# Kernel tuning notes

Hardware: AMD Instinct MI355X
Metric: run time of the kernel (lower is better)

The kernel has to match this reference:

```python
import jax, jax.numpy as jnp
import numpy as np

B, S, DIM = 2, 4096, 768
G = DIM // 3          # gate_dim = 256
H, DK = 4, G // 4     # heads=4, d_k=64
SCALE = 1.0 / np.sqrt(DK)


def setup_inputs() -> dict:
    key = jax.random.key(0)
    ks = jax.random.split(key, 9)
    r = lambda k, shp, s: (jax.random.normal(k, shp, dtype=jnp.float32) * s)
    w_s = 1.0 / np.sqrt(G)
    return {
        "x": r(ks[0], (B, S, DIM), 1.0),
        "wq": r(ks[1], (G, G), w_s), "bq": r(ks[2], (G,), 0.01),
        "wk": r(ks[3], (G, G), w_s), "bk": r(ks[4], (G,), 0.01),
        "wv": r(ks[5], (G, G), w_s), "bv": r(ks[6], (G,), 0.01),
        "wo": r(ks[7], (G, G), w_s), "bo": r(ks[8], (G,), 0.01),
    }


def reference(x, wq, bq, wk, bk, wv, bv, wo, bo):
    # chunk(3, dim=-1): q/k/v slices of width G
    xq, xk, xv = x[..., :G], x[..., G:2 * G], x[..., 2 * G:3 * G]
    # linear projections then split into heads: [b, s, h, d]
    q = (xq @ wq.T + bq).reshape(B, S, H, DK)
    k = (xk @ wk.T + bk).reshape(B, S, H, DK)
    v = (xv @ wv.T + bv).reshape(B, S, H, DK)
    scores = jnp.einsum('bihd,bjhd->bijh', q, k) * SCALE  # [b, i, j, h]
    # NOTE: original applies Softmax(dim=1) -> over the QUERY axis i
    attn = jax.nn.softmax(scores, axis=1)
    out = jnp.einsum('bijh,bjhd->bihd', attn, v).reshape(B, S, G)
    return out @ wo.T + bo
```

## Files before the change

kernel.cpp:

```cpp
#include <hip/hip_runtime.h>

#define SEQ   4096
#define HH    4
#define SCALE 0.125f
#define SC2   0.18033688011112042f
#define C16   -23.083120654223414f

typedef __bf16 bf16x8 __attribute__((ext_vector_type(8)));
typedef __bf16 bf16x4 __attribute__((ext_vector_type(4)));
typedef float  f32x4  __attribute__((ext_vector_type(4)));

constexpr size_t OFF_W16  = 0;
constexpr size_t OFF_A    = 131072;
constexpr size_t OFF_AO   = 294912;
constexpr size_t OFF_X16  = 9732096;
constexpr size_t OFF_Q16  = 12877824;
constexpr size_t K16OFF   = 2097152;
constexpr size_t V16OFF   = 4194304;
constexpr size_t OFF_PZ   = 16023552;

__device__ __forceinline__ f32x4 mf(bf16x8 a, bf16x8 b, f32x4 c) {
    return __builtin_amdgcn_mfma_f32_16x16x32_bf16(a, b, c, 0, 0, 0);
}

__device__ __forceinline__ void gload16(const __bf16* g, __bf16* l) {
    __builtin_amdgcn_global_load_lds(
        (const __attribute__((address_space(1))) unsigned int*)g,
        (__attribute__((address_space(3))) unsigned int*)l, 16, 0, 0);
}

__device__ __forceinline__ float ex2(float x) {
    return __builtin_amdgcn_exp2f(x);
}

__global__ void k_prep(const float* __restrict__ x,
                       const float* __restrict__ wq, const float* __restrict__ wk,
                       const float* __restrict__ wv, const float* __restrict__ wo,
                       float* __restrict__ ws) {
    int bx = blockIdx.x, t = threadIdx.x;
    if (bx < 6144) {
        size_t i4 = ((size_t)bx * 256 + t) * 4;
        float4 v = *(const float4*)(x + i4);
        bf16x4 o = {(__bf16)v.x, (__bf16)v.y, (__bf16)v.z, (__bf16)v.w};
        *(bf16x4*)((__bf16*)(ws + OFF_X16) + i4) = o;
    } else if (bx < 6400) {
        int q = bx - 6144;
        int y = q >> 6;
        const float* src = (y == 0) ? wq : (y == 1) ? wk : (y == 2) ? wv : wo;
        float sc = (y == 0) ? SC2 : 1.0f;
        size_t i4 = ((size_t)(q & 63) * 256 + t) * 4;
        float4 v = *(const float4*)(src + i4);
        bf16x4 o = {(__bf16)(v.x * sc), (__bf16)(v.y * sc),
                    (__bf16)(v.z * sc), (__bf16)(v.w * sc)};
        *(bf16x4*)((__bf16*)(ws + OFF_W16) + (size_t)y * 65536 + i4) = o;
    } else {
        size_t i4 = ((size_t)(bx - 6400) * 256 + t) * 4;
        *(float4*)(ws + OFF_AO + i4) = make_float4(0.f, 0.f, 0.f, 0.f);
    }
}

__global__ __launch_bounds__(256) void k_qkv_mfma(const float* __restrict__ bq,
                                                  const float* __restrict__ bk,
                                                  const float* __restrict__ bv,
                                                  float* __restrict__ ws) {
    int t = threadIdx.x, lane = t & 63, w = t >> 6;
    int yw = blockIdx.y;
    int ntb = blockIdx.z * 8;
    int row0 = blockIdx.x * 64 + w * 16;
    int mrow = lane & 15, quad = lane >> 4;
    const __bf16* X16 = (const __bf16*)(ws + OFF_X16);
    const __bf16* W16 = (const __bf16*)(ws + OFF_W16) + (size_t)yw * 65536;
    const float* bias = (yw == 0) ? bq : (yw == 1) ? bk : bv;
    __bf16* Qb = (__bf16*)(ws + OFF_Q16);
    f32x4 acc[8];
#pragma unroll
    for (int n = 0; n < 8; n++) acc[n] = {0.f, 0.f, 0.f, 0.f};
    const __bf16* ap = X16 + (size_t)(row0 + mrow) * 768 + yw * 256 + quad * 8;
    const __bf16* bp = W16 + (size_t)ntb * 4096 + (size_t)mrow * 256 + quad * 8;
    for (int kc = 0; kc < 256; kc += 32) {
        bf16x8 a = *(const bf16x8*)(ap + kc);
#pragma unroll
        for (int nt = 0; nt < 8; nt++) {
            bf16x8 b = *(const bf16x8*)(bp + (size_t)nt * 4096 + kc);
            acc[nt] = mf(a, b, acc[nt]);
        }
    }
#pragma unroll
    for (int nt = 0; nt < 8; nt++) {
        int n = (ntb + nt) * 16 + mrow;
        float bb = bias[n];
        if (yw == 0) bb *= SC2;
        int h = n >> 6, d = n & 63;
#pragma unroll
        for (int r = 0; r < 4; r++) {
            int sg = row0 + quad * 4 + r;
            int b_ = sg >> 12, s = sg & 4095;
            int bh = b_ * HH + h;
            float val = acc[nt][r] + bb;
            if (yw == 0) {
                int tile = s >> 4, m = s & 15, frag = d >> 5, q2 = (d >> 3) & 3, e = d & 7;
                size_t idx = (((size_t)bh * 256 + tile) * 2 + frag) * 512 +
                             (size_t)(q2 * 16 + m) * 8 + e;
                Qb[idx] = (__bf16)val;
            } else if (yw == 1) {
                int jc = s >> 5, jj = s & 31;
                int tl = (jj >> 2) & 1, m = ((jj >> 3) << 2) | (jj & 3);
                int frag = d >> 5, q2 = (d >> 3) & 3, e = d & 7;
                size_t idx = (((size_t)bh * 128 + jc) * 4 + tl * 2 + frag) * 512 +
                             (size_t)(q2 * 16 + m) * 8 + e;
                Qb[K16OFF + idx] = (__bf16)val;
            } else {
                int jc = s >> 5, qk = (s >> 3) & 3, e = s & 7;
                int nd = d >> 4, nl = d & 15;
                size_t idx = (((size_t)bh * 128 + jc) * 4 + nd) * 512 +
                             (size_t)(qk * 16 + nl) * 8 + e;
                Qb[V16OFF + idx] = (__bf16)val;
            }
        }
    }
}

__global__ __launch_bounds__(256) void k_colstats(float* __restrict__ ws) {
    __shared__ __bf16 qbuf[2][4096];
    int t = threadIdx.x, lane = t & 63, w = t >> 6;
    int jb = blockIdx.x, iy = blockIdx.y, bh = blockIdx.z;
    int jc0 = jb * 8 + w * 2;
    const __bf16* Qp = (const __bf16*)(ws + OFF_Q16);
    const __bf16* Kp = Qp + K16OFF;
    const __bf16* kb = Kp + ((size_t)(bh * 128 + jc0) * 4) * 512 + lane * 8;
    bf16x8 kA0 = *(const bf16x8*)(kb);
    bf16x8 kA1 = *(const bf16x8*)(kb + 512);
    bf16x8 kB0 = *(const bf16x8*)(kb + 1024);
    bf16x8 kB1 = *(const bf16x8*)(kb + 1536);
    bf16x8 kC0 = *(const bf16x8*)(kb + 2048);
    bf16x8 kC1 = *(const bf16x8*)(kb + 2560);
    bf16x8 kD0 = *(const bf16x8*)(kb + 3072);
    bf16x8 kD1 = *(const bf16x8*)(kb + 3584);
    const __bf16* q0 = Qp + ((size_t)(bh * 256 + iy * 16) * 2) * 512 +
                       w * 1024 + lane * 8;
    gload16(q0, qbuf[0] + w * 1024);
    gload16(q0 + 512, qbuf[0] + w * 1024 + 512);
    __syncthreads();
    const f32x4 cin = {C16, C16, C16, C16};
    float z0 = 0.f, z1 = 0.f, z2 = 0.f, z3 = 0.f;
    for (int ic = 0; ic < 4; ic++) {
        const __bf16* cur = qbuf[ic & 1];
        if (ic < 3) {
            const __bf16* qn = Qp + ((size_t)(bh * 256 + iy * 16 + (ic + 1) * 4) * 2) * 512 +
                               w * 1024 + lane * 8;
            gload16(qn, qbuf[(ic + 1) & 1] + w * 1024);
            gload16(qn + 512, qbuf[(ic + 1) & 1] + w * 1024 + 512);
        }
#pragma unroll
        for (int it = 0; it < 4; it++) {
            bf16x8 a0 = *(const bf16x8*)(cur + it * 1024 + lane * 8);
            bf16x8 a1 = *(const bf16x8*)(cur + it * 1024 + 512 + lane * 8);
            f32x4 cA = mf(a0, kA0, cin); cA = mf(a1, kA1, cA);
            f32x4 cB = mf(a0, kB0, cin); cB = mf(a1, kB1, cB);
            f32x4 cC = mf(a0, kC0, cin); cC = mf(a1, kC1, cC);
            f32x4 cD = mf(a0, kD0, cin); cD = mf(a1, kD1, cD);
#pragma unroll
            for (int r = 0; r < 4; r++) {
                z0 += ex2(cA[r]);
                z1 += ex2(cB[r]);
                z2 += ex2(cC[r]);
                z3 += ex2(cD[r]);
            }
        }
        __syncthreads();
    }
    z0 += __shfl_xor(z0, 16, 64);
    z0 += __shfl_xor(z0, 32, 64);
    z1 += __shfl_xor(z1, 16, 64);
    z1 += __shfl_xor(z1, 32, 64);
    z2 += __shfl_xor(z2, 16, 64);
    z2 += __shfl_xor(z2, 32, 64);
    z3 += __shfl_xor(z3, 16, 64);
    z3 += __shfl_xor(z3, 32, 64);
    if (lane < 16) {
        size_t o = OFF_PZ + (size_t)iy * 32768 + (size_t)bh * SEQ +
                   jc0 * 32 + ((lane >> 2) << 3) + (lane & 3);
        ws[o] = z0;
        ws[o + 4] = z1;
        ws[o + 32] = z2;
        ws[o + 36] = z3;
    }
}

__global__ void k_afin(float* __restrict__ ws) {
    int idx = blockIdx.x * 256 + threadIdx.x;
    const float* pz = ws + OFF_PZ;
    float Z = 0.f;
#pragma unroll
    for (int y = 0; y < 16; y++) Z += pz[(size_t)y * 32768 + idx];
    ws[OFF_A + idx] = C16 - __log2f(Z);
}

__global__ __launch_bounds__(256) void k_attnpv(float* __restrict__ ws) {
    __shared__ __align__(16) char pool[17408];
    __bf16* ldsK = (__bf16*)pool;
    __bf16* ldsV = (__bf16*)(pool + 8192);
    int t = threadIdx.x, lane = t & 63, w = t >> 6;
    int jy = blockIdx.y, bh = blockIdx.z;
    int itp = blockIdx.x * 4 + w;
    int it0 = itp * 2;
    int mrow = lane & 15, quad = lane >> 4;
    const __bf16* Qp = (const __bf16*)(ws + OFF_Q16);
    const __bf16* Kp = Qp + K16OFF;
    const __bf16* Vp = Qp + V16OFF;
    const float* Ag = ws + OFF_A + (size_t)bh * SEQ + jy * 512 + quad * 8;

    const __bf16* qb = Qp + ((size_t)(bh * 256 + it0) * 2) * 512 + lane * 8;
    bf16x8 aq00 = *(const bf16x8*)(qb);
    bf16x8 aq01 = *(const bf16x8*)(qb + 512);
    bf16x8 aq10 = *(const bf16x8*)(qb + 1024);
    bf16x8 aq11 = *(const bf16x8*)(qb + 1536);

    f32x4 oT0[4], oT1[4];
#pragma unroll
    for (int nd = 0; nd < 4; nd++) {
        oT0[nd] = {0.f, 0.f, 0.f, 0.f};
        oT1[nd] = {0.f, 0.f, 0.f, 0.f};
    }
    int c0g = jy * 16;
    const __bf16* kg = Kp + ((size_t)(bh * 128 + c0g) * 4) * 512 + w * 512 + lane * 8;
    const __bf16* vg = Vp + ((size_t)(bh * 128 + c0g) * 4) * 512 + w * 512 + lane * 8;
    gload16(kg, ldsK + w * 512);
    gload16(vg, ldsV + w * 512);
    kg += 2048; vg += 2048;
    f32x4 aL = *(const f32x4*)(Ag);
    f32x4 aH = *(const f32x4*)(Ag + 4);
    __syncthreads();

    for (int jt = 0; jt < 16; jt++) {
        const __bf16* curK = ldsK + (jt & 1) * 2048;
        const __bf16* curV = ldsV + (jt & 1) * 2048;
        f32x4 aLn = aL, aHn = aH;
        if (jt < 15) {
            gload16(kg, ldsK + ((jt + 1) & 1) * 2048 + w * 512);
            gload16(vg, ldsV + ((jt + 1) & 1) * 2048 + w * 512);
            kg += 2048; vg += 2048;
            aLn = *(const f32x4*)(Ag + (jt + 1) * 32);
            aHn = *(const f32x4*)(Ag + (jt + 1) * 32 + 4);
        }
        bf16x8 ck0 = *(const bf16x8*)(curK + lane * 8);
        bf16x8 ck1 = *(const bf16x8*)(curK + 512 + lane * 8);
        bf16x8 ck2 = *(const bf16x8*)(curK + 1024 + lane * 8);
        bf16x8 ck3 = *(const bf16x8*)(curK + 1536 + lane * 8);
        f32x4 c00 = mf(ck0, aq00, aL); c00 = mf(ck1, aq01, c00);
        f32x4 c01 = mf(ck2, aq00, aH); c01 = mf(ck3, aq01, c01);
        f32x4 c10 = mf(ck0, aq10, aL); c10 = mf(ck1, aq11, c10);
        f32x4 c11 = mf(ck2, aq10, aH); c11 = mf(ck3, aq11, c11);
        bf16x8 pb0, pb1;
#pragma unroll
        for (int r = 0; r < 4; r++) {
            pb0[r]     = (__bf16)ex2(c00[r]);
            pb0[4 + r] = (__bf16)ex2(c01[r]);
            pb1[r]     = (__bf16)ex2(c10[r]);
            pb1[4 + r] = (__bf16)ex2(c11[r]);
        }
#pragma unroll
        for (int nd = 0; nd < 4; nd++) {
            bf16x8 bv = *(const bf16x8*)(curV + nd * 512 + lane * 8);
            oT0[nd] = mf(bv, pb0, oT0[nd]);
            oT1[nd] = mf(bv, pb1, oT1[nd]);
        }
        aL = aLn; aH = aHn;
        __syncthreads();
    }

    float* sO = (float*)pool + (size_t)w * 1040;
    int b = bh >> 2, h = bh & 3;
    float* AO = ws + OFF_AO;
    int i0 = it0 * 16;
#pragma unroll
    for (int nd = 0; nd < 4; nd++)
#pragma unroll
        for (int r = 0; r < 4; r++)
            sO[mrow * 65 + nd * 16 + quad * 4 + r] = oT0[nd][r];
#pragma unroll
    for (int c = 0; c < 16; c++)
        atomicAdd(&AO[((size_t)(b * SEQ + i0 + c)) * 256 + h * 64 + lane],
                  sO[c * 65 + lane]);
#pragma unroll
    for (int nd = 0; nd < 4; nd++)
#pragma unroll
        for (int r = 0; r < 4; r++)
            sO[mrow * 65 + nd * 16 + quad * 4 + r] = oT1[nd][r];
#pragma unroll
    for (int c = 0; c < 16; c++)
        atomicAdd(&AO[((size_t)(b * SEQ + i0 + 16 + c)) * 256 + h * 64 + lane],
                  sO[c * 65 + lane]);
}

__global__ __launch_bounds__(256) void k_outproj_mfma(const float* __restrict__ bo,
                                                      float* __restrict__ ws,
                                                      float* __restrict__ out) {
    int t = threadIdx.x, lane = t & 63, w = t >> 6;
    int row0 = blockIdx.x * 64 + w * 16;
    int ntb = blockIdx.y * 4;
    int mrow = lane & 15, quad = lane >> 4;
    const float* AO = ws + OFF_AO;
    const __bf16* W16 = (const __bf16*)(ws + OFF_W16) + (size_t)3 * 65536;
    f32x4 acc[4];
#pragma unroll
    for (int n = 0; n < 4; n++) acc[n] = {0.f, 0.f, 0.f, 0.f};
    const float* ap = AO + (size_t)(row0 + mrow) * 256 + quad * 8;
    const __bf16* bp = W16 + (size_t)ntb * 4096 + (size_t)mrow * 256 + quad * 8;
    for (int kc = 0; kc < 256; kc += 32) {
        float4 u = *(const float4*)(ap + kc);
        float4 v = *(const float4*)(ap + kc + 4);
        bf16x8 a = {(__bf16)u.x, (__bf16)u.y, (__bf16)u.z, (__bf16)u.w,
                    (__bf16)v.x, (__bf16)v.y, (__bf16)v.z, (__bf16)v.w};
#pragma unroll
        for (int nt = 0; nt < 4; nt++) {
            bf16x8 b = *(const bf16x8*)(bp + (size_t)nt * 4096 + kc);
            acc[nt] = mf(a, b, acc[nt]);
        }
    }
#pragma unroll
    for (int nt = 0; nt < 4; nt++) {
        int n = (ntb + nt) * 16 + mrow;
        float bb = bo[n];
#pragma unroll
        for (int r = 0; r < 4; r++) {
            int sg = row0 + quad * 4 + r;
            out[(size_t)sg * 256 + n] = acc[nt][r] + bb;
        }
    }
}

extern "C" void kernel_launch(void* const* d_in, const int* in_sizes, int n_in,
                              void* d_out, int out_size, void* d_ws, size_t ws_size,
                              hipStream_t stream) {
    const float* x  = (const float*)d_in[0];
    const float* wq = (const float*)d_in[1];
    const float* bq = (const float*)d_in[2];
    const float* wk = (const float*)d_in[3];
    const float* bk = (const float*)d_in[4];
    const float* wv = (const float*)d_in[5];
    const float* bv = (const float*)d_in[6];
    const float* wo = (const float*)d_in[7];
    const float* bo = (const float*)d_in[8];
    float* ws = (float*)d_ws;
    float* out = (float*)d_out;

    k_prep<<<8448, 256, 0, stream>>>(x, wq, wk, wv, wo, ws);
    k_qkv_mfma<<<dim3(128, 3, 2), 256, 0, stream>>>(bq, bk, bv, ws);
    k_colstats<<<dim3(16, 16, 8), 256, 0, stream>>>(ws);
    k_afin<<<128, 256, 0, stream>>>(ws);
    k_attnpv<<<dim3(32, 8, 8), 256, 0, stream>>>(ws);
    k_outproj_mfma<<<dim3(128, 4), 256, 0, stream>>>(bo, ws, out);
}
```

Measured before the change: 220.3 us.

## Triple-buffer K/V in attention-PV with one barrier per step and larger j-chunks

The attention-PV kernel now stages K/V tiles in a three-slot LDS ring. It waits on vmcnt and uses a single s_barrier per iteration instead of double-buffering with a trailing __syncthreads. Each block processes twice as many key tiles (the grid y dimension is halved), which halves the number of atomicAdd partial-output flushes. The per-column A offsets are preloaded into LDS once rather than fetched from global memory each iteration. The tradeoffs are more LDS per block and fewer blocks, so less parallelism across the device.

```diff
diff --git a/kernel.cpp b/kernel.cpp
--- a/kernel.cpp
+++ b/kernel.cpp
@@ -197,9 +197,8 @@
 }
 
 __global__ __launch_bounds__(256) void k_attnpv(float* __restrict__ ws) {
-    __shared__ __align__(16) char pool[17408];
-    __bf16* ldsK = (__bf16*)pool;
-    __bf16* ldsV = (__bf16*)(pool + 8192);
+    __shared__ __align__(16) char pool[28672];
+    float* sA = (float*)(pool + 24576);
     int t = threadIdx.x, lane = t & 63, w = t >> 6;
     int jy = blockIdx.y, bh = blockIdx.z;
     int itp = blockIdx.x * 4 + w;
@@ -208,8 +207,11 @@
     const __bf16* Qp = (const __bf16*)(ws + OFF_Q16);
     const __bf16* Kp = Qp + K16OFF;
     const __bf16* Vp = Qp + V16OFF;
-    const float* Ag = ws + OFF_A + (size_t)bh * SEQ + jy * 512 + quad * 8;
-
+
+    {
+        const float* Ag = ws + OFF_A + (size_t)bh * SEQ + jy * 1024;
+        *(float4*)(sA + t * 4) = *(const float4*)(Ag + t * 4);
+    }
     const __bf16* qb = Qp + ((size_t)(bh * 256 + it0) * 2) * 512 + lane * 8;
     bf16x8 aq00 = *(const bf16x8*)(qb);
     bf16x8 aq01 = *(const bf16x8*)(qb + 512);
@@ -222,27 +224,30 @@
         oT0[nd] = {0.f, 0.f, 0.f, 0.f};
         oT1[nd] = {0.f, 0.f, 0.f, 0.f};
     }
-    int c0g = jy * 16;
+    int c0g = jy * 32;
     const __bf16* kg = Kp + ((size_t)(bh * 128 + c0g) * 4) * 512 + w * 512 + lane * 8;
     const __bf16* vg = Vp + ((size_t)(bh * 128 + c0g) * 4) * 512 + w * 512 + lane * 8;
-    gload16(kg, ldsK + w * 512);
-    gload16(vg, ldsV + w * 512);
+    gload16(kg, (__bf16*)pool + w * 512);
+    gload16(vg, (__bf16*)(pool + 4096) + w * 512);
     kg += 2048; vg += 2048;
-    f32x4 aL = *(const f32x4*)(Ag);
-    f32x4 aH = *(const f32x4*)(Ag + 4);
     __syncthreads();
 
-    for (int jt = 0; jt < 16; jt++) {
-        const __bf16* curK = ldsK + (jt & 1) * 2048;
-        const __bf16* curV = ldsV + (jt & 1) * 2048;
-        f32x4 aLn = aL, aHn = aH;
-        if (jt < 15) {
-            gload16(kg, ldsK + ((jt + 1) & 1) * 2048 + w * 512);
-            gload16(vg, ldsV + ((jt + 1) & 1) * 2048 + w * 512);
+    int bc = 0;
+    for (int jt = 0; jt < 32; ++jt) {
+        int bn = (bc == 2) ? 0 : bc + 1;
+        if (jt < 31) {
+            gload16(kg, (__bf16*)(pool + bn * 8192) + w * 512);
+            gload16(vg, (__bf16*)(pool + bn * 8192 + 4096) + w * 512);
             kg += 2048; vg += 2048;
-            aLn = *(const f32x4*)(Ag + (jt + 1) * 32);
-            aHn = *(const f32x4*)(Ag + (jt + 1) * 32 + 4);
-        }
+            asm volatile("s_waitcnt vmcnt(2)" ::: "memory");
+        } else {
+            asm volatile("s_waitcnt vmcnt(0)" ::: "memory");
+        }
+        __builtin_amdgcn_s_barrier();
+        const __bf16* curK = (const __bf16*)(pool + bc * 8192);
+        const __bf16* curV = (const __bf16*)(pool + bc * 8192 + 4096);
+        f32x4 aL = *(const f32x4*)(sA + jt * 32 + quad * 8);
+        f32x4 aH = *(const f32x4*)(sA + jt * 32 + quad * 8 + 4);
         bf16x8 ck0 = *(const bf16x8*)(curK + lane * 8);
         bf16x8 ck1 = *(const bf16x8*)(curK + 512 + lane * 8);
         bf16x8 ck2 = *(const bf16x8*)(curK + 1024 + lane * 8);
@@ -265,9 +270,9 @@
             oT0[nd] = mf(bv, pb0, oT0[nd]);
             oT1[nd] = mf(bv, pb1, oT1[nd]);
         }
-        aL = aLn; aH = aHn;
-        __syncthreads();
-    }
+        bc = bn;
+    }
+    __syncthreads();
 
     float* sO = (float*)pool + (size_t)w * 1040;
     int b = bh >> 2, h = bh & 3;
@@ -349,6 +354,6 @@
     k_qkv_mfma<<<dim3(128, 3, 2), 256, 0, stream>>>(bq, bk, bv, ws);
     k_colstats<<<dim3(16, 16, 8), 256, 0, stream>>>(ws);
     k_afin<<<128, 256, 0, stream>>>(ws);
-    k_attnpv<<<dim3(32, 8, 8), 256, 0, stream>>>(ws);
+    k_attnpv<<<dim3(32, 4, 8), 256, 0, stream>>>(ws);
     k_outproj_mfma<<<dim3(128, 4), 256, 0, stream>>>(bo, ws, out);
 }
```

New measurement: 204.3 us. 1.08x faster.
